# Optimization experiments

Measured on AMD Instinct MI355X. Metric: run time of the kernel, lower is better.

Reference implementation:

```python
import jax, jax.numpy as jnp
import numpy as np

N = 100000
B = 1024
NODE_DIM = 128
LATENT = 128
IN_DIM = NODE_DIM + 2 * LATENT   # 384, q/kv projection input width
FFN_IN = LATENT + IN_DIM          # 512, ffn input width


def setup_inputs() -> dict:
    key = jax.random.key(0)
    ks = jax.random.split(key, 16)
    s = 1.0 / np.sqrt(IN_DIM)
    s2 = 1.0 / np.sqrt(FFN_IN)
    s3 = 1.0 / np.sqrt(LATENT)
    return {
        "x": jax.random.normal(ks[0], (N, NODE_DIM), jnp.float32),
        "memory": jax.random.normal(ks[1], (N, LATENT), jnp.float32),
        "delta_t_vec": jax.random.normal(ks[2], (N, LATENT), jnp.float32),
        "tar_t_vec": jax.random.normal(ks[3], (B, LATENT), jnp.float32),
        # sparse neighbor mask, ~50 neighbors per target on average
        "neighbor_mask": jax.random.uniform(ks[4], (B, N)) < 5e-4,
        "tar_idx": jax.random.randint(ks[5], (B, 1), 0, N, jnp.int32),
        "Wq": jax.random.uniform(ks[6], (LATENT, IN_DIM), jnp.float32, -s, s),
        "bq": jnp.zeros((LATENT,), jnp.float32),
        "Wk": jax.random.uniform(ks[7], (LATENT, IN_DIM), jnp.float32, -s, s),
        "bk": jnp.zeros((LATENT,), jnp.float32),
        "Wv": jax.random.uniform(ks[8], (LATENT, IN_DIM), jnp.float32, -s, s),
        "bv": jnp.zeros((LATENT,), jnp.float32),
        "W1": jax.random.uniform(ks[9], (LATENT, FFN_IN), jnp.float32, -s2, s2),
        "b1": jnp.zeros((LATENT,), jnp.float32),
        "W2": jax.random.uniform(ks[10], (LATENT, LATENT), jnp.float32, -s3, s3),
        "b2": jnp.zeros((LATENT,), jnp.float32),
    }


def reference(x, memory, delta_t_vec, tar_t_vec, neighbor_mask, tar_idx,
              Wq, bq, Wk, bk, Wv, bv, W1, b1, W2, b2):
    idx = tar_idx[:, 0]                                  # [B]
    q_input = jnp.concatenate([x[idx], memory[idx], tar_t_vec], axis=-1)   # [B, IN_DIM]
    kv_input = jnp.concatenate([x, memory, delta_t_vec], axis=-1)          # [N, IN_DIM]
    q = q_input @ Wq.T + bq                              # [B, D]
    k = kv_input @ Wk.T + bk                             # [N, D]
    v = kv_input @ Wv.T + bv                             # [N, D]
    d = q.shape[-1]
    scores = jnp.einsum("bd,nd->bn", q, k) / jnp.sqrt(jnp.float32(d))      # [B, N]
    # rows with no neighbors attend to their own target node
    no_neighbor = ~jnp.any(neighbor_mask, axis=1)        # [B]
    self_mask = jnp.arange(neighbor_mask.shape[1])[None, :] == tar_idx     # [B, N]
    mask = neighbor_mask | (no_neighbor[:, None] & self_mask)
    scores = jnp.where(mask, scores, -jnp.inf)
    attn = jax.nn.softmax(scores, axis=-1)               # [B, N]
    agg = attn @ v                                       # [B, D]
    z = jnp.concatenate([agg, q_input], axis=-1)         # [B, FFN_IN]
    z = jax.nn.relu(z @ W1.T + b1) @ W2.T + b2           # [B, D]
    return z
```

## Files before the change

kernel.cpp:

```cpp
#include <hip/hip_runtime.h>
#include <stdint.h>
#include <stddef.h>

constexpr int N_NODES = 100000;
constexpr int BATCH   = 1024;
constexpr int LAT     = 128;
constexpr int INDIM   = 384;
constexpr int FFNIN   = 512;
constexpr int NB_MAX  = 512;

typedef unsigned int u32x4 __attribute__((ext_vector_type(4)));

__device__ __forceinline__ float dot4(float4 a, float4 b) {
    return a.x * b.x + a.y * b.y + a.z * b.z + a.w * b.w;
}

__global__ __launch_bounds__(384) void fused_graph_attn_kernel(
    const float* __restrict__ x,   const float* __restrict__ mem,
    const float* __restrict__ dtv, const float* __restrict__ ttv,
    const uint32_t* __restrict__ mask, const int* __restrict__ tar_idx,
    const float* __restrict__ Wq, const float* __restrict__ bq,
    const float* __restrict__ Wk, const float* __restrict__ bk,
    const float* __restrict__ Wv, const float* __restrict__ bv,
    const float* __restrict__ W1, const float* __restrict__ b1,
    const float* __restrict__ W2, const float* __restrict__ b2,
    float* __restrict__ out)
{
    const int b    = blockIdx.x;
    const int tid  = threadIdx.x;
    const int lane = tid & 63;
    const int wave = tid >> 6;

    __shared__ int cnt;
    __shared__ int jl[NB_MAX];
    __shared__ __align__(16) float qin[INDIM];
    __shared__ __align__(16) float qk[INDIM];
    __shared__ __align__(16) float u[INDIM];
    __shared__ __align__(16) float zbuf[FFNIN];
    __shared__ __align__(16) float hbuf[LAT];
    __shared__ __align__(16) float upart[6][INDIM];
    __shared__ float wm[6], ws[6], sbias_sh;

    const int idx = tar_idx[b];
    if (tid == 0) cnt = 0;

    if (tid < 128)      qin[tid] = x[(size_t)idx * LAT + tid];
    else if (tid < 256) qin[tid] = mem[(size_t)idx * LAT + (tid - 128)];
    else                qin[tid] = ttv[(size_t)b * LAT + (tid - 256)];
    __syncthreads();

    if (wave == 0) {
        const float4* qin4 = (const float4*)qin;
        const float4* r0 = (const float4*)(Wq + (size_t)lane * INDIM);
        const float4* r1 = (const float4*)(Wq + (size_t)(lane + 64) * INDIM);
        float a0 = bq[lane], a1 = bq[lane + 64];
        #pragma unroll 4
        for (int i = 0; i < INDIM / 4; ++i) {
            float4 qi = qin4[i];
            a0 += dot4(r0[i], qi);
            a1 += dot4(r1[i], qi);
        }
        float sb = a0 * bk[lane] + a1 * bk[lane + 64];
        #pragma unroll
        for (int off = 1; off < 64; off <<= 1) sb += __shfl_xor(sb, off, 64);
        if (lane == 0) sbias_sh = sb;
        float qt[6] = {0.f, 0.f, 0.f, 0.f, 0.f, 0.f};
        for (int l = 0; l < 64; ++l) {
            float qd = __shfl(a0, l, 64);
            const float* wkp = Wk + (size_t)l * INDIM + lane;
            #pragma unroll
            for (int t = 0; t < 6; ++t) qt[t] += qd * wkp[64 * t];
        }
        for (int l = 0; l < 64; ++l) {
            float qd = __shfl(a1, l, 64);
            const float* wkp = Wk + (size_t)(l + 64) * INDIM + lane;
            #pragma unroll
            for (int t = 0; t < 6; ++t) qt[t] += qd * wkp[64 * t];
        }
        #pragma unroll
        for (int t = 0; t < 6; ++t) qk[lane + 64 * t] = qt[t];
    } else {
        const u32x4* row = (const u32x4*)(mask + (size_t)b * N_NODES);
        #pragma unroll 2
        for (int i = tid - 64; i < N_NODES / 4; i += 320) {
            u32x4 v = __builtin_nontemporal_load(row + i);
            if (v.x | v.y | v.z | v.w) {
                uint32_t w[4] = {v.x, v.y, v.z, v.w};
                #pragma unroll
                for (int wi = 0; wi < 4; ++wi) {
                    if (w[wi]) {
                        int slot = atomicAdd(&cnt, 1);
                        if (slot < NB_MAX) jl[slot] = i * 4 + wi;
                    }
                }
            }
        }
    }
    __syncthreads();
    if (tid == 0 && cnt == 0) { jl[0] = idx; cnt = 1; }
    __syncthreads();
    const int nb = cnt < NB_MAX ? cnt : NB_MAX;

    const float scale = 0.088388347648318447f;
    const float sb = sbias_sh;
    float qkr[6];
    #pragma unroll
    for (int k = 0; k < 6; ++k) qkr[k] = qk[lane + 64 * k];

    float m = -INFINITY, ssum = 0.f;
    float ua[6] = {0.f, 0.f, 0.f, 0.f, 0.f, 0.f};
    for (int jj = wave; jj < nb; jj += 6) {
        const int j = jl[jj];
        const float* xp = x   + (size_t)j * LAT;
        const float* mp = mem + (size_t)j * LAT;
        const float* dp = dtv + (size_t)j * LAT;
        const float f0 = xp[lane], f1 = xp[lane + 64];
        const float f2 = mp[lane], f3 = mp[lane + 64];
        const float f4 = dp[lane], f5 = dp[lane + 64];
        float p = qkr[0] * f0 + qkr[1] * f1 + qkr[2] * f2
                + qkr[3] * f3 + qkr[4] * f4 + qkr[5] * f5;
        #pragma unroll
        for (int off = 1; off < 64; off <<= 1) p += __shfl_xor(p, off, 64);
        const float s    = (p + sb) * scale;
        const float mn   = fmaxf(m, s);
        const float corr = __expf(m - mn);
        const float e    = __expf(s - mn);
        ssum = ssum * corr + e;
        ua[0] = ua[0] * corr + e * f0;  ua[1] = ua[1] * corr + e * f1;
        ua[2] = ua[2] * corr + e * f2;  ua[3] = ua[3] * corr + e * f3;
        ua[4] = ua[4] * corr + e * f4;  ua[5] = ua[5] * corr + e * f5;
        m = mn;
    }
    if (lane == 0) { wm[wave] = m; ws[wave] = ssum; }
    #pragma unroll
    for (int k = 0; k < 6; ++k) upart[wave][lane + 64 * k] = ua[k];
    __syncthreads();

    {
        float mstar = wm[0];
        #pragma unroll
        for (int w = 1; w < 6; ++w) mstar = fmaxf(mstar, wm[w]);
        float num = 0.f, den = 0.f;
        #pragma unroll
        for (int w = 0; w < 6; ++w) {
            const float c = __expf(wm[w] - mstar);
            num += c * upart[w][tid];
            den += c * ws[w];
        }
        u[tid] = num / den;
    }
    __syncthreads();

    float* part = &upart[0][0];
    const int o  = tid & 127;
    const int pp = tid >> 7;

    {
        const float4* wr = (const float4*)(Wv + (size_t)o * INDIM);
        const float4* uv = (const float4*)u;
        const int i0 = pp * 32;
        float acc = 0.f;
        #pragma unroll 4
        for (int i = i0; i < i0 + 32; ++i) acc += dot4(wr[i], uv[i]);
        part[pp * 128 + o] = acc;
    }
    zbuf[LAT + tid] = qin[tid];
    __syncthreads();
    if (tid < 128) zbuf[tid] = bv[tid] + part[tid] + part[128 + tid] + part[256 + tid];
    __syncthreads();

    {
        const float4* wr = (const float4*)(W1 + (size_t)o * FFNIN);
        const float4* zv = (const float4*)zbuf;
        const int i0 = pp * 43;
        const int i1 = (pp == 2) ? 128 : i0 + 43;
        float acc = 0.f;
        #pragma unroll 4
        for (int i = i0; i < i1; ++i) acc += dot4(wr[i], zv[i]);
        part[pp * 128 + o] = acc;
    }
    __syncthreads();
    if (tid < 128)
        hbuf[tid] = fmaxf(b1[tid] + part[tid] + part[128 + tid] + part[256 + tid], 0.f);
    __syncthreads();

    {
        const float4* wr = (const float4*)(W2 + (size_t)o * LAT);
        const float4* hv = (const float4*)hbuf;
        const int i0 = pp * 11;
        const int i1 = (pp == 2) ? 32 : i0 + 11;
        float acc = 0.f;
        #pragma unroll 4
        for (int i = i0; i < i1; ++i) acc += dot4(wr[i], hv[i]);
        part[pp * 128 + o] = acc;
    }
    __syncthreads();
    if (tid < 128)
        out[(size_t)b * LAT + tid] = b2[tid] + part[tid] + part[128 + tid] + part[256 + tid];
}

extern "C" void kernel_launch(void* const* d_in, const int* in_sizes, int n_in,
                              void* d_out, int out_size, void* d_ws, size_t ws_size,
                              hipStream_t stream) {
    const float*    x    = (const float*)d_in[0];
    const float*    mem  = (const float*)d_in[1];
    const float*    dtv  = (const float*)d_in[2];
    const float*    ttv  = (const float*)d_in[3];
    const uint32_t* mask = (const uint32_t*)d_in[4];
    const int*      tidx = (const int*)d_in[5];
    const float*    Wq   = (const float*)d_in[6];
    const float*    bq   = (const float*)d_in[7];
    const float*    Wk   = (const float*)d_in[8];
    const float*    bk   = (const float*)d_in[9];
    const float*    Wv   = (const float*)d_in[10];
    const float*    bv   = (const float*)d_in[11];
    const float*    W1   = (const float*)d_in[12];
    const float*    b1   = (const float*)d_in[13];
    const float*    W2   = (const float*)d_in[14];
    const float*    b2   = (const float*)d_in[15];
    float* out = (float*)d_out;

    fused_graph_attn_kernel<<<BATCH, 384, 0, stream>>>(
        x, mem, dtv, ttv, mask, tidx, Wq, bq, Wk, bk, Wv, bv, W1, b1, W2, b2,
        out);
}
```

Baseline: 687.3 us.

## Scan mask with all waves and compute q/qk projection block-wide afterward

Previously wave 0 computed the q projection and q·Wk serially while the other five waves scanned the 400KB mask row. Now all six waves scan the mask, with four independent nontemporal loads issued per iteration. The q and qk projections then run across all 384 threads after the scan. This raises memory-level parallelism on the dominant mask read, but gives up overlapping the projection with the scan and adds two barriers.

```diff
diff --git a/kernel.cpp b/kernel.cpp
--- a/kernel.cpp
+++ b/kernel.cpp
@@ -8,6 +8,7 @@
 constexpr int INDIM   = 384;
 constexpr int FFNIN   = 512;
 constexpr int NB_MAX  = 512;
+constexpr int NV      = N_NODES / 4;
 
 typedef unsigned int u32x4 __attribute__((ext_vector_type(4)));
 
@@ -34,6 +35,7 @@
     __shared__ int cnt;
     __shared__ int jl[NB_MAX];
     __shared__ __align__(16) float qin[INDIM];
+    __shared__ __align__(16) float qv[LAT];
     __shared__ __align__(16) float qk[INDIM];
     __shared__ __align__(16) float u[INDIM];
     __shared__ __align__(16) float zbuf[FFNIN];
@@ -49,57 +51,71 @@
     else                qin[tid] = ttv[(size_t)b * LAT + (tid - 256)];
     __syncthreads();
 
-    if (wave == 0) {
-        const float4* qin4 = (const float4*)qin;
-        const float4* r0 = (const float4*)(Wq + (size_t)lane * INDIM);
-        const float4* r1 = (const float4*)(Wq + (size_t)(lane + 64) * INDIM);
-        float a0 = bq[lane], a1 = bq[lane + 64];
-        #pragma unroll 4
-        for (int i = 0; i < INDIM / 4; ++i) {
-            float4 qi = qin4[i];
-            a0 += dot4(r0[i], qi);
-            a1 += dot4(r1[i], qi);
-        }
-        float sb = a0 * bk[lane] + a1 * bk[lane + 64];
-        #pragma unroll
-        for (int off = 1; off < 64; off <<= 1) sb += __shfl_xor(sb, off, 64);
-        if (lane == 0) sbias_sh = sb;
-        float qt[6] = {0.f, 0.f, 0.f, 0.f, 0.f, 0.f};
-        for (int l = 0; l < 64; ++l) {
-            float qd = __shfl(a0, l, 64);
-            const float* wkp = Wk + (size_t)l * INDIM + lane;
-            #pragma unroll
-            for (int t = 0; t < 6; ++t) qt[t] += qd * wkp[64 * t];
-        }
-        for (int l = 0; l < 64; ++l) {
-            float qd = __shfl(a1, l, 64);
-            const float* wkp = Wk + (size_t)(l + 64) * INDIM + lane;
-            #pragma unroll
-            for (int t = 0; t < 6; ++t) qt[t] += qd * wkp[64 * t];
-        }
-        #pragma unroll
-        for (int t = 0; t < 6; ++t) qk[lane + 64 * t] = qt[t];
-    } else {
+    {
         const u32x4* row = (const u32x4*)(mask + (size_t)b * N_NODES);
-        #pragma unroll 2
-        for (int i = tid - 64; i < N_NODES / 4; i += 320) {
-            u32x4 v = __builtin_nontemporal_load(row + i);
+        auto proc = [&](u32x4 v, int base) {
             if (v.x | v.y | v.z | v.w) {
                 uint32_t w[4] = {v.x, v.y, v.z, v.w};
                 #pragma unroll
                 for (int wi = 0; wi < 4; ++wi) {
                     if (w[wi]) {
                         int slot = atomicAdd(&cnt, 1);
-                        if (slot < NB_MAX) jl[slot] = i * 4 + wi;
+                        if (slot < NB_MAX) jl[slot] = base * 4 + wi;
                     }
                 }
             }
+        };
+        int i = tid;
+        for (; i + 3 * 384 < NV; i += 4 * 384) {
+            u32x4 v0 = __builtin_nontemporal_load(row + i);
+            u32x4 v1 = __builtin_nontemporal_load(row + i + 384);
+            u32x4 v2 = __builtin_nontemporal_load(row + i + 768);
+            u32x4 v3 = __builtin_nontemporal_load(row + i + 1152);
+            proc(v0, i);
+            proc(v1, i + 384);
+            proc(v2, i + 768);
+            proc(v3, i + 1152);
         }
+        for (; i < NV; i += 384) {
+            u32x4 v = __builtin_nontemporal_load(row + i);
+            proc(v, i);
+        }
     }
     __syncthreads();
     if (tid == 0 && cnt == 0) { jl[0] = idx; cnt = 1; }
     __syncthreads();
     const int nb = cnt < NB_MAX ? cnt : NB_MAX;
+
+    float* part = &upart[0][0];
+    const int o  = tid & 127;
+    const int pp = tid >> 7;
+
+    {
+        const float4* wr  = (const float4*)(Wq + (size_t)o * INDIM);
+        const float4* qi4 = (const float4*)qin;
+        const int i0 = pp * 32;
+        float acc = 0.f;
+        #pragma unroll 4
+        for (int i = i0; i < i0 + 32; ++i) acc += dot4(wr[i], qi4[i]);
+        part[pp * 128 + o] = acc;
+    }
+    __syncthreads();
+    if (tid < 128) qv[tid] = bq[tid] + part[tid] + part[128 + tid] + part[256 + tid];
+    __syncthreads();
+
+    {
+        float acc = 0.f;
+        #pragma unroll 8
+        for (int d = 0; d < LAT; ++d) acc += qv[d] * Wk[(size_t)d * INDIM + tid];
+        qk[tid] = acc;
+    }
+    if (wave == 0) {
+        float p = qv[lane] * bk[lane] + qv[lane + 64] * bk[lane + 64];
+        #pragma unroll
+        for (int off = 1; off < 64; off <<= 1) p += __shfl_xor(p, off, 64);
+        if (lane == 0) sbias_sh = p;
+    }
+    __syncthreads();
 
     const float scale = 0.088388347648318447f;
     const float sb = sbias_sh;
@@ -150,10 +166,6 @@
         u[tid] = num / den;
     }
     __syncthreads();
-
-    float* part = &upart[0][0];
-    const int o  = tid & 127;
-    const int pp = tid >> 7;
 
     {
         const float4* wr = (const float4*)(Wv + (size_t)o * INDIM);
```

New measurement: 684.4 us. No clear change (-0.4%).
